# Performance work log

Hardware: AMD Instinct MI355X
Metric: run time of the kernel (lower is better)

Reference implementation:

```python
import jax, jax.numpy as jnp
import numpy as np
from jax.ops import segment_sum

N = 100000      # nodes
E = 1600000     # edges (avg degree 16)
F_IN = 100      # data.num_features
D1 = 64         # dim1
D2 = 64         # dim2
CONV = 4        # conv_count
FC = 2          # fc_count
G = 500         # graphs in batch


def setup_inputs() -> dict:
    key = jax.random.key(0)
    ks = jax.random.split(key, 16)
    inp = {}
    inp['x'] = jax.random.normal(ks[0], (N, F_IN), dtype=jnp.float32)
    inp['edge_index'] = jax.random.randint(ks[1], (2, E), 0, N, dtype=jnp.int64)
    inp['edge_weight'] = jax.random.uniform(ks[2], (E,), dtype=jnp.float32)
    inp['batch'] = jnp.sort(jax.random.randint(ks[3], (N,), 0, G, dtype=jnp.int64))
    s = 0.05
    inp['lin0_w'] = jax.random.normal(ks[4], (F_IN, D1), dtype=jnp.float32) * s
    inp['lin0_b'] = jnp.zeros((D1,), dtype=jnp.float32)
    inp['conv_w'] = jax.random.normal(ks[5], (CONV, D1, D1), dtype=jnp.float32) * s
    inp['conv_b'] = jnp.zeros((CONV, D1), dtype=jnp.float32)
    inp['lin1_w'] = jax.random.normal(ks[6], (D1, D2), dtype=jnp.float32) * s
    inp['lin1_b'] = jnp.zeros((D2,), dtype=jnp.float32)
    inp['fc_w'] = jax.random.normal(ks[7], (FC, D2, D2), dtype=jnp.float32) * s
    inp['fc_b'] = jnp.zeros((FC, D2), dtype=jnp.float32)
    inp['lin2_w'] = jax.random.normal(ks[8], (D2, 1), dtype=jnp.float32) * s
    inp['lin2_b'] = jnp.zeros((1,), dtype=jnp.float32)
    return inp


def reference(x, edge_index, edge_weight, batch,
              lin0_w, lin0_b, conv_w, conv_b,
              lin1_w, lin1_b, fc_w, fc_b, lin2_w, lin2_b):
    row, col = edge_index[0], edge_index[1]  # source -> target

    # GCN symmetric normalization (add_self_loops=False, so 'improved' is a no-op)
    deg = segment_sum(edge_weight, col, num_segments=N)          # [N]
    dis = jnp.where(deg > 0, jax.lax.rsqrt(deg), 0.0)            # deg^{-1/2}, inf->0
    norm = dis[row] * edge_weight * dis[col]                     # [E]

    out = jax.nn.relu(x @ lin0_w + lin0_b)                       # [N, D1]
    for i in range(CONV):
        h = out @ conv_w[i]                                      # [N, D1]
        msg = h[row] * norm[:, None]                             # gather + scale, [E, D1]
        agg = segment_sum(msg, col, num_segments=N)              # scatter-add, [N, D1]
        out = jax.nn.relu(agg + conv_b[i])

    # global_mean_pool over graph ids
    sums = segment_sum(out, batch, num_segments=G)               # [G, D1]
    cnt = segment_sum(jnp.ones((N,), dtype=out.dtype), batch, num_segments=G)
    pooled = sums / jnp.clip(cnt, 1.0)[:, None]

    out = jax.nn.relu(pooled @ lin1_w + lin1_b)                  # [G, D2]
    for i in range(FC):
        out = jax.nn.relu(out @ fc_w[i] + fc_b[i])
    out = out @ lin2_w + lin2_b                                  # [G, 1]
    return out.reshape(-1)                                       # [G]
```

## Files before the change

### kernel.cpp

```cpp
#include <hip/hip_runtime.h>

#define NN 100000
#define NE 1600000
#define FIN 100
#define D 64
#define NCONV 4
#define NG 500

#define NB 196
#define BSH 9
#define EPB 4096
#define NBLKA ((NE + EPB - 1) / EPB)
#define NSCAN (NB * NBLKA)
#define SB 512
#define NBLKS ((NSCAN + SB - 1) / SB)

#define LSTR 136
#define ASTR 72

typedef unsigned int uint;
typedef unsigned short ushort;
typedef __attribute__((ext_vector_type(8))) short bf16x8;
typedef __attribute__((ext_vector_type(4))) float f32x4;

__device__ inline ushort f2bf(float x) {
    uint u = __float_as_uint(x);
    u += 0x7fffu + ((u >> 16) & 1u);
    return (ushort)(u >> 16);
}
__device__ inline float bflo(uint u) { return __uint_as_float(u << 16); }
__device__ inline float bfhi(uint u) { return __uint_as_float(u & 0xffff0000u); }
__device__ inline float bf2f(ushort s) { return __uint_as_float((uint)s << 16); }

__global__ __launch_bounds__(256) void k_hist(const int* __restrict__ col,
                                              int* __restrict__ ghist) {
    __shared__ int lh[NB];
    int t = threadIdx.x;
    if (t < NB) lh[t] = 0;
    __syncthreads();
    int base = blockIdx.x * EPB;
    #pragma unroll
    for (int i = 0; i < 16; ++i) {
        int e = base + i * 256 + t;
        if (e < NE) atomicAdd(&lh[col[e] >> BSH], 1);
    }
    __syncthreads();
    if (t < NB) ghist[t * NBLKA + blockIdx.x] = lh[t];
}

__global__ __launch_bounds__(SB) void s_scan1(const int* __restrict__ in,
                                              int* __restrict__ out,
                                              int* __restrict__ bsums, int n) {
    __shared__ int sh[SB];
    int t = threadIdx.x, i = blockIdx.x * SB + t;
    int v = (i < n) ? in[i] : 0;
    sh[t] = v;
    __syncthreads();
    for (int off = 1; off < SB; off <<= 1) {
        int u = (t >= off) ? sh[t - off] : 0;
        __syncthreads();
        sh[t] += u;
        __syncthreads();
    }
    if (i < n) out[i] = sh[t] - v;
    if (t == SB - 1) bsums[blockIdx.x] = sh[t];
}

__global__ __launch_bounds__(SB) void s_scan2(int* __restrict__ bsums, int nb) {
    __shared__ int sh[SB];
    int t = threadIdx.x;
    int v = (t < nb) ? bsums[t] : 0;
    sh[t] = v;
    __syncthreads();
    for (int off = 1; off < SB; off <<= 1) {
        int u = (t >= off) ? sh[t - off] : 0;
        __syncthreads();
        sh[t] += u;
        __syncthreads();
    }
    if (t < nb) bsums[t] = sh[t] - v;
}

__global__ __launch_bounds__(SB) void s_scan3(int* __restrict__ out,
                                              const int* __restrict__ bsums, int n) {
    int i = blockIdx.x * SB + threadIdx.x;
    if (i < n) out[i] += bsums[blockIdx.x];
}

__global__ __launch_bounds__(256) void k_scatter(const int* __restrict__ row,
                                                 const int* __restrict__ col,
                                                 const float* __restrict__ ew,
                                                 const int* __restrict__ gscan,
                                                 int2* __restrict__ sorted) {
    __shared__ int lcur[NB];
    int t = threadIdx.x;
    if (t < NB) lcur[t] = gscan[t * NBLKA + blockIdx.x];
    __syncthreads();
    int base = blockIdx.x * EPB;
    #pragma unroll
    for (int i = 0; i < 16; ++i) {
        int e = base + i * 256 + t;
        if (e < NE) {
            int c = col[e];
            int pos = atomicAdd(&lcur[c >> BSH], 1);
            sorted[pos] = make_int2(row[e] | ((c & 511) << 17), __float_as_int(ew[e]));
        }
    }
}

__global__ __launch_bounds__(SB) void k_bcsr(const int2* __restrict__ sorted,
                                             const int* __restrict__ gscan,
                                             int* __restrict__ rowstart,
                                             int2* __restrict__ csr,
                                             float* __restrict__ dis) {
    __shared__ int lcnt[SB];
    __shared__ int lscan[SB];
    __shared__ float ldeg[SB];
    int t = threadIdx.x, b = blockIdx.x;
    int base = gscan[b * NBLKA];
    int end  = (b == NB - 1) ? NE : gscan[(b + 1) * NBLKA];
    lcnt[t] = 0;
    ldeg[t] = 0.f;
    __syncthreads();
    for (int e = base + t; e < end; e += SB) {
        int2 p = sorted[e];
        int c = p.x >> 17;
        atomicAdd(&lcnt[c], 1);
        atomicAdd(&ldeg[c], __int_as_float(p.y));
    }
    __syncthreads();
    int v = lcnt[t];
    lscan[t] = v;
    __syncthreads();
    for (int off = 1; off < SB; off <<= 1) {
        int u = (t >= off) ? lscan[t - off] : 0;
        __syncthreads();
        lscan[t] += u;
        __syncthreads();
    }
    int ex = lscan[t] - v;
    int idx = b * SB + t;
    if (idx <= NN) rowstart[idx] = base + ex;
    if (idx < NN) {
        float dd = ldeg[t];
        dis[idx] = (dd > 0.f) ? (1.0f / sqrtf(dd)) : 0.f;
    }
    lcnt[t] = base + ex;
    __syncthreads();
    for (int e = base + t; e < end; e += SB) {
        int2 p = sorted[e];
        int slot = atomicAdd(&lcnt[p.x >> 17], 1);
        csr[slot] = make_int2(p.x & 0x1FFFF, p.y);
    }
}

__global__ __launch_bounds__(256) void k_rownorm(int2* __restrict__ csr,
                                                 const int* __restrict__ rowstart,
                                                 const float* __restrict__ dis) {
    int t = threadIdx.x;
    int node = blockIdx.x * 16 + (t >> 4);
    int f = t & 15;
    int e0 = rowstart[node], e1 = rowstart[node + 1];
    float dc = dis[node];
    for (int e = e0 + f; e < e1; e += 16) {
        int2 p = csr[e];
        float w = dis[p.x] * __int_as_float(p.y) * dc;
        csr[e] = make_int2(p.x, __float_as_int(w));
    }
}

__global__ void k_wsplit_all(const float* __restrict__ conv_w,
                             const float* __restrict__ lin0_w,
                             ushort* __restrict__ wf, ushort* __restrict__ wf0) {
    int tid = blockIdx.x * blockDim.x + threadIdx.x;
    if (tid < 16384) {
        int j = tid & 7;
        int lane = (tid >> 3) & 63;
        int kh = (tid >> 9) & 1;
        int ct = (tid >> 10) & 3;
        int l = tid >> 12;
        int k = kh * 32 + (lane >> 4) * 8 + j;
        int n = ct * 16 + (lane & 15);
        float w = conv_w[l * D * D + k * D + n];
        ushort hi = f2bf(w);
        ushort lo = f2bf(w - bf2f(hi));
        int base = (((l * 4 + ct) * 2 + kh) * 2) * 512 + lane * 8 + j;
        wf[base] = hi;
        wf[base + 512] = lo;
    } else {
        int s = tid - 16384;
        int j = s & 7;
        int lane = (s >> 3) & 63;
        int ks = (s >> 9) & 3;
        int ct = s >> 11;
        int k = ks * 32 + (lane >> 4) * 8 + j;
        int n = ct * 16 + (lane & 15);
        float v = (k < FIN) ? lin0_w[k * D + n] : 0.f;
        ushort hi = f2bf(v);
        ushort lo = f2bf(v - bf2f(hi));
        int base = ((ct * 4 + ks) * 2) * 512 + lane * 8 + j;
        wf0[base] = hi;
        wf0[base + 512] = lo;
    }
}

__global__ __launch_bounds__(256) void k_lin0_mfma(const float* __restrict__ x,
                                                   const ushort* __restrict__ wf,
                                                   const float* __restrict__ b,
                                                   ushort* __restrict__ out) {
    __shared__ ushort xhi[64 * LSTR];
    int t = threadIdx.x;
    int r0 = blockIdx.x * 64;
    for (int i = t; i < 1600; i += 256) {
        int r = i / 25, c4 = i - (i / 25) * 25;
        float4 v = {0.f, 0.f, 0.f, 0.f};
        if (r0 + r < NN)
            v = *reinterpret_cast<const float4*>(&x[(size_t)(r0 + r) * FIN + c4 * 4]);
        int base = r * LSTR + c4 * 4;
        xhi[base + 0] = f2bf(v.x);
        xhi[base + 1] = f2bf(v.y);
        xhi[base + 2] = f2bf(v.z);
        xhi[base + 3] = f2bf(v.w);
    }
    for (int i = t; i < 64 * 28; i += 256) {
        int r = i / 28, c = FIN + (i - (i / 28) * 28);
        xhi[r * LSTR + c] = 0;
    }
    __syncthreads();
    int wave = t >> 6, lane = t & 63;
    int lrow = wave * 16 + (lane & 15);
    bf16x8 ahi[4];
    #pragma unroll
    for (int ks = 0; ks < 4; ++ks) {
        int off = lrow * LSTR + ks * 32 + (lane >> 4) * 8;
        ahi[ks] = *reinterpret_cast<const bf16x8*>(&xhi[off]);
    }
    float bv[4];
    #pragma unroll
    for (int ct = 0; ct < 4; ++ct) bv[ct] = b[ct * 16 + (lane & 15)];
    int r = r0 + wave * 16;
    f32x4 acc[4];
    #pragma unroll
    for (int ct = 0; ct < 4; ++ct) {
        acc[ct] = {bv[ct], bv[ct], bv[ct], bv[ct]};
        #pragma unroll
        for (int ks = 0; ks < 4; ++ks) {
            int base = ((ct * 4 + ks) * 2) * 512 + lane * 8;
            bf16x8 wh = *reinterpret_cast<const bf16x8*>(&wf[base]);
            bf16x8 wl = *reinterpret_cast<const bf16x8*>(&wf[base + 512]);
            acc[ct] = __builtin_amdgcn_mfma_f32_16x16x32_bf16(ahi[ks], wh, acc[ct], 0, 0, 0);
            acc[ct] = __builtin_amdgcn_mfma_f32_16x16x32_bf16(ahi[ks], wl, acc[ct], 0, 0, 0);
        }
    }
    #pragma unroll
    for (int ct = 0; ct < 4; ++ct) {
        int ocol = ct * 16 + (lane & 15);
        #pragma unroll
        for (int i = 0; i < 4; ++i) {
            int orow = r + (lane >> 4) * 4 + i;
            if (orow < NN) out[orow * D + ocol] = f2bf(fmaxf(acc[ct][i], 0.f));
        }
    }
}

__global__ __launch_bounds__(256, 8) void k_conv_fused(const ushort* __restrict__ src,
                                                       const int* __restrict__ rowstart,
                                                       const int2* __restrict__ csr,
                                                       const ushort* __restrict__ wf,
                                                       const float* __restrict__ bias,
                                                       ushort* __restrict__ dst) {
    __shared__ ushort arow[4][16 * ASTR];
    int t = threadIdx.x;
    int wave = t >> 6, lane = t & 63;
    int g = lane >> 4;
    int f = lane & 15;
    int n0 = blockIdx.x * 64 + wave * 16;
    if (n0 >= NN) return;
    ushort* tile = arow[wave];

    #pragma unroll
    for (int p = 0; p < 4; ++p) {
        int rloc = p * 4 + g;
        int node = n0 + rloc;
        int e0 = rowstart[node], e1 = rowstart[node + 1];
        float4 acc = {0.f, 0.f, 0.f, 0.f};
        int2 p0, p1, p2, p3;
        {
            int a0 = e0 + 0 < e1 ? e0 + 0 : 0;
            int a1 = e0 + 1 < e1 ? e0 + 1 : 0;
            int a2 = e0 + 2 < e1 ? e0 + 2 : 0;
            int a3 = e0 + 3 < e1 ? e0 + 3 : 0;
            p0 = csr[a0]; p1 = csr[a1]; p2 = csr[a2]; p3 = csr[a3];
        }
        for (int base = e0; base < e1; base += 4) {
            int n0e = base + 4 < e1 ? base + 4 : 0;
            int n1e = base + 5 < e1 ? base + 5 : 0;
            int n2e = base + 6 < e1 ? base + 6 : 0;
            int n3e = base + 7 < e1 ? base + 7 : 0;
            int2 q0 = csr[n0e], q1 = csr[n1e], q2 = csr[n2e], q3 = csr[n3e];
            float w0 = (base + 0 < e1) ? __int_as_float(p0.y) : 0.f;
            float w1 = (base + 1 < e1) ? __int_as_float(p1.y) : 0.f;
            float w2 = (base + 2 < e1) ? __int_as_float(p2.y) : 0.f;
            float w3 = (base + 3 < e1) ? __int_as_float(p3.y) : 0.f;
            uint2 v0 = *reinterpret_cast<const uint2*>(&src[p0.x * D + f * 4]);
            uint2 v1 = *reinterpret_cast<const uint2*>(&src[p1.x * D + f * 4]);
            uint2 v2 = *reinterpret_cast<const uint2*>(&src[p2.x * D + f * 4]);
            uint2 v3 = *reinterpret_cast<const uint2*>(&src[p3.x * D + f * 4]);
            acc.x = fmaf(bflo(v0.x), w0, acc.x); acc.y = fmaf(bfhi(v0.x), w0, acc.y);
            acc.z = fmaf(bflo(v0.y), w0, acc.z); acc.w = fmaf(bfhi(v0.y), w0, acc.w);
            acc.x = fmaf(bflo(v1.x), w1, acc.x); acc.y = fmaf(bfhi(v1.x), w1, acc.y);
            acc.z = fmaf(bflo(v1.y), w1, acc.z); acc.w = fmaf(bfhi(v1.y), w1, acc.w);
            acc.x = fmaf(bflo(v2.x), w2, acc.x); acc.y = fmaf(bfhi(v2.x), w2, acc.y);
            acc.z = fmaf(bflo(v2.y), w2, acc.z); acc.w = fmaf(bfhi(v2.y), w2, acc.w);
            acc.x = fmaf(bflo(v3.x), w3, acc.x); acc.y = fmaf(bfhi(v3.x), w3, acc.y);
            acc.z = fmaf(bflo(v3.y), w3, acc.z); acc.w = fmaf(bfhi(v3.y), w3, acc.w);
            p0 = q0; p1 = q1; p2 = q2; p3 = q3;
        }
        uint2 o;
        o.x = (uint)f2bf(acc.x) | ((uint)f2bf(acc.y) << 16);
        o.y = (uint)f2bf(acc.z) | ((uint)f2bf(acc.w) << 16);
        *reinterpret_cast<uint2*>(&tile[rloc * ASTR + f * 4]) = o;
    }
    int arow_idx = lane & 15;
    bf16x8 a0 = *reinterpret_cast<const bf16x8*>(&tile[arow_idx * ASTR + (lane >> 4) * 8]);
    bf16x8 a1 = *reinterpret_cast<const bf16x8*>(&tile[arow_idx * ASTR + 32 + (lane >> 4) * 8]);
    #pragma unroll
    for (int ct = 0; ct < 4; ++ct) {
        int base0 = ((ct * 2 + 0) * 2) * 512 + lane * 8;
        int base1 = ((ct * 2 + 1) * 2) * 512 + lane * 8;
        bf16x8 wh0 = *reinterpret_cast<const bf16x8*>(&wf[base0]);
        bf16x8 wl0 = *reinterpret_cast<const bf16x8*>(&wf[base0 + 512]);
        bf16x8 wh1 = *reinterpret_cast<const bf16x8*>(&wf[base1]);
        bf16x8 wl1 = *reinterpret_cast<const bf16x8*>(&wf[base1 + 512]);
        float bv = bias[ct * 16 + (lane & 15)];
        f32x4 c = {bv, bv, bv, bv};
        c = __builtin_amdgcn_mfma_f32_16x16x32_bf16(a0, wh0, c, 0, 0, 0);
        c = __builtin_amdgcn_mfma_f32_16x16x32_bf16(a1, wh1, c, 0, 0, 0);
        c = __builtin_amdgcn_mfma_f32_16x16x32_bf16(a0, wl0, c, 0, 0, 0);
        c = __builtin_amdgcn_mfma_f32_16x16x32_bf16(a1, wl1, c, 0, 0, 0);
        int ocol = ct * 16 + (lane & 15);
        #pragma unroll
        for (int i = 0; i < 4; ++i) {
            int orow = n0 + (lane >> 4) * 4 + i;
            dst[orow * D + ocol] = f2bf(fmaxf(c[i], 0.f));
        }
    }
}

__global__ __launch_bounds__(256) void k_pool(const ushort* __restrict__ src,
                                              const int* __restrict__ batch,
                                              float* __restrict__ pooled,
                                              float* __restrict__ cnt) {
    int wave = threadIdx.x >> 6, lane = threadIdx.x & 63;
    int n0 = blockIdx.x * 64 + wave * 16;
    float s = 0.f;
    int curg = -1, runlen = 0;
    for (int i = 0; i < 16; ++i) {
        int node = n0 + i;
        if (node >= NN) break;
        int gg = batch[node];
        if (gg != curg) {
            if (curg >= 0) {
                atomicAdd(&pooled[curg * D + lane], s);
                if (lane == 0) atomicAdd(&cnt[curg], (float)runlen);
            }
            curg = gg; s = 0.f; runlen = 0;
        }
        s += bf2f(src[node * D + lane]);
        ++runlen;
    }
    if (curg >= 0) {
        atomicAdd(&pooled[curg * D + lane], s);
        if (lane == 0) atomicAdd(&cnt[curg], (float)runlen);
    }
}

__global__ __launch_bounds__(64) void k_head(const float* __restrict__ pooled,
                                             const float* __restrict__ cnt,
                                             const float* __restrict__ lin1_w,
                                             const float* __restrict__ lin1_b,
                                             const float* __restrict__ fc_w,
                                             const float* __restrict__ fc_b,
                                             const float* __restrict__ lin2_w,
                                             const float* __restrict__ lin2_b,
                                             float* __restrict__ out) {
    __shared__ float buf0[D], buf1[D];
    int g = blockIdx.x, d = threadIdx.x;
    float c = fmaxf(cnt[g], 1.0f);
    buf0[d] = pooled[g * D + d] / c;
    __syncthreads();
    float acc = lin1_b[d];
    #pragma unroll
    for (int k = 0; k < D; ++k) acc += buf0[k] * lin1_w[k * D + d];
    buf1[d] = fmaxf(acc, 0.f);
    __syncthreads();
    acc = fc_b[d];
    #pragma unroll
    for (int k = 0; k < D; ++k) acc += buf1[k] * fc_w[k * D + d];
    buf0[d] = fmaxf(acc, 0.f);
    __syncthreads();
    acc = fc_b[D + d];
    #pragma unroll
    for (int k = 0; k < D; ++k) acc += buf0[k] * fc_w[D * D + k * D + d];
    buf1[d] = fmaxf(acc, 0.f);
    __syncthreads();
    float v = buf1[d] * lin2_w[d];
    #pragma unroll
    for (int off = 32; off; off >>= 1) v += __shfl_down(v, off);
    if (d == 0) out[g] = v + lin2_b[0];
}

extern "C" void kernel_launch(void* const* d_in, const int* in_sizes, int n_in,
                              void* d_out, int out_size, void* d_ws, size_t ws_size,
                              hipStream_t stream) {
    const float* x      = (const float*)d_in[0];
    const int*   ei     = (const int*)  d_in[1];
    const float* ew     = (const float*)d_in[2];
    const int*   batch  = (const int*)  d_in[3];
    const float* lin0_w = (const float*)d_in[4];
    const float* lin0_b = (const float*)d_in[5];
    const float* conv_w = (const float*)d_in[6];
    const float* conv_b = (const float*)d_in[7];
    const float* lin1_w = (const float*)d_in[8];
    const float* lin1_b = (const float*)d_in[9];
    const float* fc_w   = (const float*)d_in[10];
    const float* fc_b   = (const float*)d_in[11];
    const float* lin2_w = (const float*)d_in[12];
    const float* lin2_b = (const float*)d_in[13];
    float* out = (float*)d_out;

    const int* rowv = ei;
    const int* colv = ei + NE;

    ushort* bufA    = (ushort*)d_ws;
    ushort* bufB    = bufA + (size_t)NN * D;
    ushort* bufG    = bufB + (size_t)NN * D;
    int2*   csr     = (int2*)(bufG + (size_t)NN * D);
    int*   rowstart = (int*)(csr + NE);
    float* dis      = (float*)(rowstart + NN + 1);
    float* pooled   = dis + NN;
    float* cnt      = pooled + NG * D;
    ushort* wfrags  = (ushort*)(cnt + NG);
    ushort* wfrags0 = wfrags + 4 * 8192;
    int2*  sorted   = (int2*)bufG;
    int*   ghist    = (int*)bufB;
    int*   gscan    = ghist + NSCAN;
    int*   bsums    = gscan + NSCAN;

    hipMemsetAsync(pooled, 0, (NG * D + NG) * sizeof(float), stream);

    k_hist<<<NBLKA, 256, 0, stream>>>(colv, ghist);
    s_scan1<<<NBLKS, SB, 0, stream>>>(ghist, gscan, bsums, NSCAN);
    s_scan2<<<1, SB, 0, stream>>>(bsums, NBLKS);
    s_scan3<<<NBLKS, SB, 0, stream>>>(gscan, bsums, NSCAN);
    k_scatter<<<NBLKA, 256, 0, stream>>>(rowv, colv, ew, gscan, sorted);
    k_bcsr<<<NB, SB, 0, stream>>>(sorted, gscan, rowstart, csr, dis);

    k_rownorm<<<NN / 16, 256, 0, stream>>>(csr, rowstart, dis);
    k_wsplit_all<<<96, 256, 0, stream>>>(conv_w, lin0_w, wfrags, wfrags0);

    k_lin0_mfma<<<(NN + 63) / 64, 256, 0, stream>>>(x, wfrags0, lin0_b, bufA);

    int cg = (NN + 63) / 64;
    k_conv_fused<<<cg, 256, 0, stream>>>(bufA, rowstart, csr, wfrags + 0 * 8192,
                                         conv_b + 0 * D, bufB);
    k_conv_fused<<<cg, 256, 0, stream>>>(bufB, rowstart, csr, wfrags + 1 * 8192,
                                         conv_b + 1 * D, bufA);
    k_conv_fused<<<cg, 256, 0, stream>>>(bufA, rowstart, csr, wfrags + 2 * 8192,
                                         conv_b + 2 * D, bufB);
    k_conv_fused<<<cg, 256, 0, stream>>>(bufB, rowstart, csr, wfrags + 3 * 8192,
                                         conv_b + 3 * D, bufA);

    k_pool<<<(NN + 63) / 64, 256, 0, stream>>>(bufA, batch, pooled, cnt);
    k_head<<<NG, 64, 0, stream>>>(pooled, cnt, lin1_w, lin1_b, fc_w, fc_b,
                                  lin2_w, lin2_b, out);
}
```

Measured before the change: 311.0 us.

## Split conv kernel work: one node per 16-lane group, one column tile per wave

The fused conv kernel previously had each wave gather 16 nodes sequentially (4 passes of 4 nodes) and then compute all four output column tiles with MFMA. Now each block covers 16 nodes. Each 16-lane group gathers one node, the results are shared through LDS after a block barrier, and each wave computes one 16-column MFMA tile. This gives four times more blocks and more independent gathers in flight, aimed at hiding gather latency, at the cost of a __syncthreads and more blocks per launch.

```diff
diff --git a/kernel.cpp b/kernel.cpp
--- a/kernel.cpp
+++ b/kernel.cpp
@@ -269,81 +269,74 @@
                                                        const ushort* __restrict__ wf,
                                                        const float* __restrict__ bias,
                                                        ushort* __restrict__ dst) {
-    __shared__ ushort arow[4][16 * ASTR];
+    __shared__ ushort arow[16 * ASTR];
     int t = threadIdx.x;
     int wave = t >> 6, lane = t & 63;
     int g = lane >> 4;
     int f = lane & 15;
-    int n0 = blockIdx.x * 64 + wave * 16;
-    if (n0 >= NN) return;
-    ushort* tile = arow[wave];
-
-    #pragma unroll
-    for (int p = 0; p < 4; ++p) {
-        int rloc = p * 4 + g;
-        int node = n0 + rloc;
-        int e0 = rowstart[node], e1 = rowstart[node + 1];
-        float4 acc = {0.f, 0.f, 0.f, 0.f};
-        int2 p0, p1, p2, p3;
-        {
-            int a0 = e0 + 0 < e1 ? e0 + 0 : 0;
-            int a1 = e0 + 1 < e1 ? e0 + 1 : 0;
-            int a2 = e0 + 2 < e1 ? e0 + 2 : 0;
-            int a3 = e0 + 3 < e1 ? e0 + 3 : 0;
-            p0 = csr[a0]; p1 = csr[a1]; p2 = csr[a2]; p3 = csr[a3];
-        }
-        for (int base = e0; base < e1; base += 4) {
-            int n0e = base + 4 < e1 ? base + 4 : 0;
-            int n1e = base + 5 < e1 ? base + 5 : 0;
-            int n2e = base + 6 < e1 ? base + 6 : 0;
-            int n3e = base + 7 < e1 ? base + 7 : 0;
-            int2 q0 = csr[n0e], q1 = csr[n1e], q2 = csr[n2e], q3 = csr[n3e];
-            float w0 = (base + 0 < e1) ? __int_as_float(p0.y) : 0.f;
-            float w1 = (base + 1 < e1) ? __int_as_float(p1.y) : 0.f;
-            float w2 = (base + 2 < e1) ? __int_as_float(p2.y) : 0.f;
-            float w3 = (base + 3 < e1) ? __int_as_float(p3.y) : 0.f;
-            uint2 v0 = *reinterpret_cast<const uint2*>(&src[p0.x * D + f * 4]);
-            uint2 v1 = *reinterpret_cast<const uint2*>(&src[p1.x * D + f * 4]);
-            uint2 v2 = *reinterpret_cast<const uint2*>(&src[p2.x * D + f * 4]);
-            uint2 v3 = *reinterpret_cast<const uint2*>(&src[p3.x * D + f * 4]);
-            acc.x = fmaf(bflo(v0.x), w0, acc.x); acc.y = fmaf(bfhi(v0.x), w0, acc.y);
-            acc.z = fmaf(bflo(v0.y), w0, acc.z); acc.w = fmaf(bfhi(v0.y), w0, acc.w);
-            acc.x = fmaf(bflo(v1.x), w1, acc.x); acc.y = fmaf(bfhi(v1.x), w1, acc.y);
-            acc.z = fmaf(bflo(v1.y), w1, acc.z); acc.w = fmaf(bfhi(v1.y), w1, acc.w);
-            acc.x = fmaf(bflo(v2.x), w2, acc.x); acc.y = fmaf(bfhi(v2.x), w2, acc.y);
-            acc.z = fmaf(bflo(v2.y), w2, acc.z); acc.w = fmaf(bfhi(v2.y), w2, acc.w);
-            acc.x = fmaf(bflo(v3.x), w3, acc.x); acc.y = fmaf(bfhi(v3.x), w3, acc.y);
-            acc.z = fmaf(bflo(v3.y), w3, acc.z); acc.w = fmaf(bfhi(v3.y), w3, acc.w);
-            p0 = q0; p1 = q1; p2 = q2; p3 = q3;
-        }
-        uint2 o;
-        o.x = (uint)f2bf(acc.x) | ((uint)f2bf(acc.y) << 16);
-        o.y = (uint)f2bf(acc.z) | ((uint)f2bf(acc.w) << 16);
-        *reinterpret_cast<uint2*>(&tile[rloc * ASTR + f * 4]) = o;
-    }
+    int rloc = wave * 4 + g;
+    int node = blockIdx.x * 16 + rloc;
+    int e0 = rowstart[node], e1 = rowstart[node + 1];
+    float4 acc = {0.f, 0.f, 0.f, 0.f};
+    int2 p0, p1, p2, p3;
+    {
+        int a0 = e0 + 0 < e1 ? e0 + 0 : 0;
+        int a1 = e0 + 1 < e1 ? e0 + 1 : 0;
+        int a2 = e0 + 2 < e1 ? e0 + 2 : 0;
+        int a3 = e0 + 3 < e1 ? e0 + 3 : 0;
+        p0 = csr[a0]; p1 = csr[a1]; p2 = csr[a2]; p3 = csr[a3];
+    }
+    for (int base = e0; base < e1; base += 4) {
+        int n0 = base + 4 < e1 ? base + 4 : 0;
+        int n1 = base + 5 < e1 ? base + 5 : 0;
+        int n2 = base + 6 < e1 ? base + 6 : 0;
+        int n3 = base + 7 < e1 ? base + 7 : 0;
+        int2 q0 = csr[n0], q1 = csr[n1], q2 = csr[n2], q3 = csr[n3];
+        float w0 = (base + 0 < e1) ? __int_as_float(p0.y) : 0.f;
+        float w1 = (base + 1 < e1) ? __int_as_float(p1.y) : 0.f;
+        float w2 = (base + 2 < e1) ? __int_as_float(p2.y) : 0.f;
+        float w3 = (base + 3 < e1) ? __int_as_float(p3.y) : 0.f;
+        uint2 v0 = *reinterpret_cast<const uint2*>(&src[p0.x * D + f * 4]);
+        uint2 v1 = *reinterpret_cast<const uint2*>(&src[p1.x * D + f * 4]);
+        uint2 v2 = *reinterpret_cast<const uint2*>(&src[p2.x * D + f * 4]);
+        uint2 v3 = *reinterpret_cast<const uint2*>(&src[p3.x * D + f * 4]);
+        acc.x = fmaf(bflo(v0.x), w0, acc.x); acc.y = fmaf(bfhi(v0.x), w0, acc.y);
+        acc.z = fmaf(bflo(v0.y), w0, acc.z); acc.w = fmaf(bfhi(v0.y), w0, acc.w);
+        acc.x = fmaf(bflo(v1.x), w1, acc.x); acc.y = fmaf(bfhi(v1.x), w1, acc.y);
+        acc.z = fmaf(bflo(v1.y), w1, acc.z); acc.w = fmaf(bfhi(v1.y), w1, acc.w);
+        acc.x = fmaf(bflo(v2.x), w2, acc.x); acc.y = fmaf(bfhi(v2.x), w2, acc.y);
+        acc.z = fmaf(bflo(v2.y), w2, acc.z); acc.w = fmaf(bfhi(v2.y), w2, acc.w);
+        acc.x = fmaf(bflo(v3.x), w3, acc.x); acc.y = fmaf(bfhi(v3.x), w3, acc.y);
+        acc.z = fmaf(bflo(v3.y), w3, acc.z); acc.w = fmaf(bfhi(v3.y), w3, acc.w);
+        p0 = q0; p1 = q1; p2 = q2; p3 = q3;
+    }
+    uint2 o;
+    o.x = (uint)f2bf(acc.x) | ((uint)f2bf(acc.y) << 16);
+    o.y = (uint)f2bf(acc.z) | ((uint)f2bf(acc.w) << 16);
+    *reinterpret_cast<uint2*>(&arow[rloc * ASTR + f * 4]) = o;
+    __syncthreads();
+    int ct = wave;
+    int base0 = ((ct * 2 + 0) * 2) * 512 + lane * 8;
+    int base1 = ((ct * 2 + 1) * 2) * 512 + lane * 8;
+    bf16x8 wh0 = *reinterpret_cast<const bf16x8*>(&wf[base0]);
+    bf16x8 wl0 = *reinterpret_cast<const bf16x8*>(&wf[base0 + 512]);
+    bf16x8 wh1 = *reinterpret_cast<const bf16x8*>(&wf[base1]);
+    bf16x8 wl1 = *reinterpret_cast<const bf16x8*>(&wf[base1 + 512]);
     int arow_idx = lane & 15;
-    bf16x8 a0 = *reinterpret_cast<const bf16x8*>(&tile[arow_idx * ASTR + (lane >> 4) * 8]);
-    bf16x8 a1 = *reinterpret_cast<const bf16x8*>(&tile[arow_idx * ASTR + 32 + (lane >> 4) * 8]);
-    #pragma unroll
-    for (int ct = 0; ct < 4; ++ct) {
-        int base0 = ((ct * 2 + 0) * 2) * 512 + lane * 8;
-        int base1 = ((ct * 2 + 1) * 2) * 512 + lane * 8;
-        bf16x8 wh0 = *reinterpret_cast<const bf16x8*>(&wf[base0]);
-        bf16x8 wl0 = *reinterpret_cast<const bf16x8*>(&wf[base0 + 512]);
-        bf16x8 wh1 = *reinterpret_cast<const bf16x8*>(&wf[base1]);
-        bf16x8 wl1 = *reinterpret_cast<const bf16x8*>(&wf[base1 + 512]);
-        float bv = bias[ct * 16 + (lane & 15)];
-        f32x4 c = {bv, bv, bv, bv};
-        c = __builtin_amdgcn_mfma_f32_16x16x32_bf16(a0, wh0, c, 0, 0, 0);
-        c = __builtin_amdgcn_mfma_f32_16x16x32_bf16(a1, wh1, c, 0, 0, 0);
-        c = __builtin_amdgcn_mfma_f32_16x16x32_bf16(a0, wl0, c, 0, 0, 0);
-        c = __builtin_amdgcn_mfma_f32_16x16x32_bf16(a1, wl1, c, 0, 0, 0);
-        int ocol = ct * 16 + (lane & 15);
-        #pragma unroll
-        for (int i = 0; i < 4; ++i) {
-            int orow = n0 + (lane >> 4) * 4 + i;
-            dst[orow * D + ocol] = f2bf(fmaxf(c[i], 0.f));
-        }
+    bf16x8 a0 = *reinterpret_cast<const bf16x8*>(&arow[arow_idx * ASTR + (lane >> 4) * 8]);
+    bf16x8 a1 = *reinterpret_cast<const bf16x8*>(&arow[arow_idx * ASTR + 32 + (lane >> 4) * 8]);
+    float bv = bias[ct * 16 + (lane & 15)];
+    f32x4 c = {bv, bv, bv, bv};
+    c = __builtin_amdgcn_mfma_f32_16x16x32_bf16(a0, wh0, c, 0, 0, 0);
+    c = __builtin_amdgcn_mfma_f32_16x16x32_bf16(a1, wh1, c, 0, 0, 0);
+    c = __builtin_amdgcn_mfma_f32_16x16x32_bf16(a0, wl0, c, 0, 0, 0);
+    c = __builtin_amdgcn_mfma_f32_16x16x32_bf16(a1, wl1, c, 0, 0, 0);
+    int ocol = ct * 16 + (lane & 15);
+    int r0 = blockIdx.x * 16;
+    #pragma unroll
+    for (int i = 0; i < 4; ++i) {
+        int orow = r0 + (lane >> 4) * 4 + i;
+        dst[orow * D + ocol] = f2bf(fmaxf(c[i], 0.f));
     }
 }
 
@@ -461,7 +454,7 @@
 
     k_lin0_mfma<<<(NN + 63) / 64, 256, 0, stream>>>(x, wfrags0, lin0_b, bufA);
 
-    int cg = (NN + 63) / 64;
+    int cg = NN / 16;
     k_conv_fused<<<cg, 256, 0, stream>>>(bufA, rowstart, csr, wfrags + 0 * 8192,
                                          conv_b + 0 * D, bufB);
     k_conv_fused<<<cg, 256, 0, stream>>>(bufB, rowstart, csr, wfrags + 1 * 8192,
```

Result: faster. 281.7 us, median of 2 (-9.4%).
